# Performance work log

Measured on AMD Instinct MI355X. Metric: run time of the kernel, lower is better.

Reference implementation:

```python
import jax, jax.numpy as jnp
import numpy as np

B, T, D = 128, 2048, 256

def setup_inputs() -> dict:
    key = jax.random.key(0)
    k1, k2, k3, k4, k5 = jax.random.split(key, 5)
    h = jax.random.normal(k1, (B, D), dtype=jnp.float32)
    h_traj = jax.random.normal(k2, (B, T, D), dtype=jnp.float32)
    mask = jax.random.randint(k3, (B, T), 0, 2).astype(bool)  # True = masked
    # Linear(dim, 1) params (torch default init: U(-1/sqrt(D), 1/sqrt(D)))
    bound = 1.0 / np.sqrt(D)
    w = jax.random.uniform(k4, (D,), minval=-bound, maxval=bound, dtype=jnp.float32)
    b = jax.random.uniform(k5, (), minval=-bound, maxval=bound, dtype=jnp.float32)
    return {"h": h, "h_traj": h_traj, "mask": mask, "w": w, "b": b}

def reference(h, h_traj, mask, w, b):
    # score_bt = l1(h * h_traj) : broadcast multiply then dim->1 linear
    scores = jnp.einsum("bd,btd,d->bt", h, h_traj, w) + b          # [B, T]
    scores = jnp.where(mask, -jnp.inf, scores)
    beta = jax.nn.softmax(scores, axis=1)                           # [B, T]
    z = jnp.einsum("bt,btd->bd", beta, h_traj)                      # [B, D]
    return z
```

## Files before the change

### kernel.cpp

```cpp
#include <hip/hip_runtime.h>
#include <cstdint>

#define BB 128
#define TT 2048
#define DD 256
#define NCHUNK 8
#define TC (TT / NCHUNK)
#define NPART (BB * NCHUNK)


__global__ __launch_bounds__(256) void soft_att_partial(
    const float* __restrict__ h,
    const float* __restrict__ htraj,
    const int*   __restrict__ mask,
    const float* __restrict__ w,
    const float* __restrict__ bias,
    float* __restrict__ msv,
    float* __restrict__ lsv,
    float* __restrict__ zsv)
{
    const int blk  = blockIdx.x;
    const int b    = blk / NCHUNK;
    const int c    = blk % NCHUNK;
    const int tid  = threadIdx.x;
    const int lane = tid & 63;
    const int wv   = tid >> 6;
    const int g    = lane >> 4;
    const int i    = lane & 15;
    const int grp  = tid >> 4;

    const float* hb = h + (size_t)b * DD + i * 4;
    const float* wb = w + i * 4;
    float4 hw0, hw1, hw2, hw3;
    {
        float4 h0 = *(const float4*)(hb);       float4 w0 = *(const float4*)(wb);
        float4 h1 = *(const float4*)(hb + 64);  float4 w1 = *(const float4*)(wb + 64);
        float4 h2 = *(const float4*)(hb + 128); float4 w2 = *(const float4*)(wb + 128);
        float4 h3 = *(const float4*)(hb + 192); float4 w3 = *(const float4*)(wb + 192);
        hw0 = make_float4(h0.x*w0.x, h0.y*w0.y, h0.z*w0.z, h0.w*w0.w);
        hw1 = make_float4(h1.x*w1.x, h1.y*w1.y, h1.z*w1.z, h1.w*w1.w);
        hw2 = make_float4(h2.x*w2.x, h2.y*w2.y, h2.z*w2.z, h2.w*w2.w);
        hw3 = make_float4(h3.x*w3.x, h3.y*w3.y, h3.z*w3.z, h3.w*w3.w);
    }
    const float bscal = bias[0];

    const int t0 = c * TC + wv * 64;
    const int mk = mask[(size_t)b * TT + t0 + lane];
    unsigned long long bits = __ballot(mk == 0);

    const float* rowbase = htraj + ((size_t)b * TT + t0) * DD + i * 4;

    float m = -3.0e38f, l = 0.0f;
    float4 a0 = make_float4(0,0,0,0), a1 = a0, a2 = a0, a3 = a0;

    const int n = (int)((__popcll(bits) + 3) >> 2);

#define POP(r_, ok_) { \
    unsigned long long b0_ = bits; \
    unsigned long long b1_ = b0_ & (b0_ - 1); \
    unsigned long long b2_ = b1_ & (b1_ - 1); \
    unsigned long long b3_ = b2_ & (b2_ - 1); \
    int r0_ = b0_ ? __builtin_ctzll(b0_) : 0; \
    int r1_ = b1_ ? __builtin_ctzll(b1_) : 0; \
    int r2_ = b2_ ? __builtin_ctzll(b2_) : 0; \
    int r3_ = b3_ ? __builtin_ctzll(b3_) : 0; \
    bits = b3_ & (b3_ - 1); \
    r_  = (g & 2) ? ((g & 1) ? r3_ : r2_) : ((g & 1) ? r1_ : r0_); \
    ok_ = (g & 2) ? ((g & 1) ? (b3_ != 0) : (b2_ != 0)) \
                  : ((g & 1) ? (b1_ != 0) : (b0_ != 0)); }

#define LOADV(V0_, V1_, V2_, V3_, r_, ok_) { \
    if (ok_) { const float* p_ = rowbase + (size_t)(r_) * DD; \
        V0_ = *(const float4*)(p_); \
        V1_ = *(const float4*)(p_ + 64); \
        V2_ = *(const float4*)(p_ + 128); \
        V3_ = *(const float4*)(p_ + 192); } }

#define PROC(V0_, V1_, V2_, V3_, ok_) { \
    float s0_ = V0_.x*hw0.x; s0_ = fmaf(V0_.y,hw0.y,s0_); s0_ = fmaf(V0_.z,hw0.z,s0_); s0_ = fmaf(V0_.w,hw0.w,s0_); \
    float s1_ = V1_.x*hw1.x; s1_ = fmaf(V1_.y,hw1.y,s1_); s1_ = fmaf(V1_.z,hw1.z,s1_); s1_ = fmaf(V1_.w,hw1.w,s1_); \
    float s2_ = V2_.x*hw2.x; s2_ = fmaf(V2_.y,hw2.y,s2_); s2_ = fmaf(V2_.z,hw2.z,s2_); s2_ = fmaf(V2_.w,hw2.w,s2_); \
    float s3_ = V3_.x*hw3.x; s3_ = fmaf(V3_.y,hw3.y,s3_); s3_ = fmaf(V3_.z,hw3.z,s3_); s3_ = fmaf(V3_.w,hw3.w,s3_); \
    float s_ = (s0_ + s1_) + (s2_ + s3_); \
    s_ += __shfl_xor(s_, 1, 64); \
    s_ += __shfl_xor(s_, 2, 64); \
    s_ += __shfl_xor(s_, 4, 64); \
    s_ += __shfl_xor(s_, 8, 64); \
    s_ = (ok_) ? s_ + bscal : -INFINITY; \
    float mn_ = fmaxf(m, s_); \
    float sc_ = __expf(m - mn_); \
    float p_  = __expf(s_ - mn_); \
    a0.x = fmaf(a0.x, sc_, p_*V0_.x); a0.y = fmaf(a0.y, sc_, p_*V0_.y); \
    a0.z = fmaf(a0.z, sc_, p_*V0_.z); a0.w = fmaf(a0.w, sc_, p_*V0_.w); \
    a1.x = fmaf(a1.x, sc_, p_*V1_.x); a1.y = fmaf(a1.y, sc_, p_*V1_.y); \
    a1.z = fmaf(a1.z, sc_, p_*V1_.z); a1.w = fmaf(a1.w, sc_, p_*V1_.w); \
    a2.x = fmaf(a2.x, sc_, p_*V2_.x); a2.y = fmaf(a2.y, sc_, p_*V2_.y); \
    a2.z = fmaf(a2.z, sc_, p_*V2_.z); a2.w = fmaf(a2.w, sc_, p_*V2_.w); \
    a3.x = fmaf(a3.x, sc_, p_*V3_.x); a3.y = fmaf(a3.y, sc_, p_*V3_.y); \
    a3.z = fmaf(a3.z, sc_, p_*V3_.z); a3.w = fmaf(a3.w, sc_, p_*V3_.w); \
    l = fmaf(l, sc_, p_); m = mn_; }

    float4 A0 = make_float4(0,0,0,0), A1 = A0, A2 = A0, A3 = A0;
    float4 B0 = A0, B1 = A0, B2 = A0, B3 = A0;
    bool okA = false, okB = false;

    if (n > 0) { int r; POP(r, okA); LOADV(A0, A1, A2, A3, r, okA); }
    int it = 0;
    while (it < n) {
        if (it + 1 < n) { int r; POP(r, okB); LOADV(B0, B1, B2, B3, r, okB); }
        PROC(A0, A1, A2, A3, okA);
        if (++it >= n) break;
        if (it + 1 < n) { int r; POP(r, okA); LOADV(A0, A1, A2, A3, r, okA); }
        PROC(B0, B1, B2, B3, okB);
        if (++it >= n) break;
    }

    __shared__ float sm[16];
    __shared__ float sl[16];
    __shared__ float sz[16][DD];

    *(float4*)&sz[grp][i * 4      ] = a0;
    *(float4*)&sz[grp][i * 4 + 64 ] = a1;
    *(float4*)&sz[grp][i * 4 + 128] = a2;
    *(float4*)&sz[grp][i * 4 + 192] = a3;
    if (i == 0) { sm[grp] = m; sl[grp] = l; }
    __syncthreads();

    float M = -3.0e38f;
    #pragma unroll
    for (int k = 0; k < 16; ++k) M = fmaxf(M, sm[k]);
    float L = 0.f, Z = 0.f;
    #pragma unroll
    for (int k = 0; k < 16; ++k) {
        float e = __expf(sm[k] - M);
        L = fmaf(sl[k], e, L);
        Z = fmaf(sz[k][tid], e, Z);
    }
    if (tid == 0) { msv[blk] = M; lsv[blk] = L; }
    zsv[(size_t)blk * DD + tid] = Z;
#undef POP
#undef LOADV
#undef PROC
}

__global__ __launch_bounds__(128) void soft_att_combine(
    const float* __restrict__ msv,
    const float* __restrict__ lsv,
    const float* __restrict__ zsv,
    float* __restrict__ out)
{
    const int blk = blockIdx.x;
    const int b   = blk >> 1;
    const int d   = ((blk & 1) << 7) + threadIdx.x;

    float M = -3.0e38f;
    #pragma unroll
    for (int p = 0; p < NCHUNK; ++p)
        M = fmaxf(M, msv[b * NCHUNK + p]);

    float L = 0.f, Z = 0.f;
    #pragma unroll
    for (int p = 0; p < NCHUNK; ++p) {
        float e = __expf(msv[b * NCHUNK + p] - M);
        L = fmaf(lsv[b * NCHUNK + p], e, L);
        Z = fmaf(zsv[(size_t)(b * NCHUNK + p) * DD + d], e, Z);
    }
    out[(size_t)b * DD + d] = Z / L;
}

extern "C" void kernel_launch(void* const* d_in, const int* in_sizes, int n_in,
                              void* d_out, int out_size, void* d_ws, size_t ws_size,
                              hipStream_t stream) {
    const float* h     = (const float*)d_in[0];
    const float* htraj = (const float*)d_in[1];
    const int*   mask  = (const int*)d_in[2];
    const float* w     = (const float*)d_in[3];
    const float* bias  = (const float*)d_in[4];
    float* out = (float*)d_out;

    float* ms = (float*)d_ws;
    float* ls = ms + NPART;
    float* zs = ls + NPART;

    soft_att_partial<<<dim3(BB * NCHUNK), dim3(256), 0, stream>>>(
        h, htraj, mask, w, bias, ms, ls, zs);
    soft_att_combine<<<dim3(BB * 2), dim3(128), 0, stream>>>(ms, ls, zs, out);
}
```

Baseline: 30.80 us.

## Balance unmasked rows across all 16 groups via shared-memory compacted row lists

Instead of each wave popping bits from its own 64-row ballot, the block builds a compacted list of unmasked rows across all 256 rows in shared memory, interleaved so each of the 16 row-groups gets an equal share. This balances work across waves when mask density differs per wave and removes the per-iteration bit-popping arithmetic. It adds two block-level barriers and shared-memory prefix computation before the main loop.

```diff
diff --git a/kernel.cpp b/kernel.cpp
--- a/kernel.cpp
+++ b/kernel.cpp
@@ -8,6 +8,12 @@
 #define TC (TT / NCHUNK)
 #define NPART (BB * NCHUNK)
 
+
+__device__ __forceinline__ int rowOf(const uint4& lw, int s) {
+    unsigned word = (s & 8) ? ((s & 4) ? lw.w : lw.z)
+                            : ((s & 4) ? lw.y : lw.x);
+    return (int)((word >> ((s & 3) * 8)) & 255u);
+}
 
 __global__ __launch_bounds__(256) void soft_att_partial(
     const float* __restrict__ h,
@@ -25,7 +31,6 @@
     const int tid  = threadIdx.x;
     const int lane = tid & 63;
     const int wv   = tid >> 6;
-    const int g    = lane >> 4;
     const int i    = lane & 15;
     const int grp  = tid >> 4;
 
@@ -44,33 +49,39 @@
     }
     const float bscal = bias[0];
 
-    const int t0 = c * TC + wv * 64;
-    const int mk = mask[(size_t)b * TT + t0 + lane];
-    unsigned long long bits = __ballot(mk == 0);
-
-    const float* rowbase = htraj + ((size_t)b * TT + t0) * DD + i * 4;
+    __shared__ unsigned long long wballot[4];
+    __shared__ unsigned char lists[16][16];
+    __shared__ float sm[16];
+    __shared__ float sl[16];
+    __shared__ float sz[16][DD];
+
+    const int row = tid;
+    const int mk  = mask[(size_t)b * TT + c * TC + row];
+    unsigned long long bt = __ballot(mk == 0);
+    if (lane == 0) wballot[wv] = bt;
+    __syncthreads();
+    int prev = 0, tot = 0;
+    #pragma unroll
+    for (int k = 0; k < 4; ++k) {
+        int pc = __popcll(wballot[k]);
+        prev += (k < wv) ? pc : 0;
+        tot  += pc;
+    }
+    const int rank = prev + __popcll(bt & ((1ull << lane) - 1ull));
+    if (mk == 0) lists[rank & 15][rank >> 4] = (unsigned char)row;
+    __syncthreads();
+
+    const int cntmax = (tot + 15) >> 4;
+    const int mycnt  = (tot > grp) ? ((tot - grp + 15) >> 4) : 0;
+    const uint4 lw = *(const uint4*)&lists[grp][0];
+
+    const float* chunkbase = htraj + ((size_t)b * TT + c * TC) * DD + i * 4;
 
     float m = -3.0e38f, l = 0.0f;
     float4 a0 = make_float4(0,0,0,0), a1 = a0, a2 = a0, a3 = a0;
 
-    const int n = (int)((__popcll(bits) + 3) >> 2);
-
-#define POP(r_, ok_) { \
-    unsigned long long b0_ = bits; \
-    unsigned long long b1_ = b0_ & (b0_ - 1); \
-    unsigned long long b2_ = b1_ & (b1_ - 1); \
-    unsigned long long b3_ = b2_ & (b2_ - 1); \
-    int r0_ = b0_ ? __builtin_ctzll(b0_) : 0; \
-    int r1_ = b1_ ? __builtin_ctzll(b1_) : 0; \
-    int r2_ = b2_ ? __builtin_ctzll(b2_) : 0; \
-    int r3_ = b3_ ? __builtin_ctzll(b3_) : 0; \
-    bits = b3_ & (b3_ - 1); \
-    r_  = (g & 2) ? ((g & 1) ? r3_ : r2_) : ((g & 1) ? r1_ : r0_); \
-    ok_ = (g & 2) ? ((g & 1) ? (b3_ != 0) : (b2_ != 0)) \
-                  : ((g & 1) ? (b1_ != 0) : (b0_ != 0)); }
-
 #define LOADV(V0_, V1_, V2_, V3_, r_, ok_) { \
-    if (ok_) { const float* p_ = rowbase + (size_t)(r_) * DD; \
+    if (ok_) { const float* p_ = chunkbase + (size_t)(r_) * DD; \
         V0_ = *(const float4*)(p_); \
         V1_ = *(const float4*)(p_ + 64); \
         V2_ = *(const float4*)(p_ + 128); \
@@ -102,22 +113,24 @@
 
     float4 A0 = make_float4(0,0,0,0), A1 = A0, A2 = A0, A3 = A0;
     float4 B0 = A0, B1 = A0, B2 = A0, B3 = A0;
-    bool okA = false, okB = false;
-
-    if (n > 0) { int r; POP(r, okA); LOADV(A0, A1, A2, A3, r, okA); }
+
+    bool okA = (0 < mycnt), okB = false;
+    if (okA) { int r = rowOf(lw, 0); LOADV(A0, A1, A2, A3, r, okA); }
     int it = 0;
-    while (it < n) {
-        if (it + 1 < n) { int r; POP(r, okB); LOADV(B0, B1, B2, B3, r, okB); }
+    while (it < cntmax) {
+        if (it + 1 < cntmax) {
+            okB = (it + 1 < mycnt);
+            if (okB) { int r = rowOf(lw, it + 1); LOADV(B0, B1, B2, B3, r, okB); }
+        }
         PROC(A0, A1, A2, A3, okA);
-        if (++it >= n) break;
-        if (it + 1 < n) { int r; POP(r, okA); LOADV(A0, A1, A2, A3, r, okA); }
+        if (++it >= cntmax) break;
+        if (it + 1 < cntmax) {
+            okA = (it + 1 < mycnt);
+            if (okA) { int r = rowOf(lw, it + 1); LOADV(A0, A1, A2, A3, r, okA); }
+        }
         PROC(B0, B1, B2, B3, okB);
-        if (++it >= n) break;
-    }
-
-    __shared__ float sm[16];
-    __shared__ float sl[16];
-    __shared__ float sz[16][DD];
+        ++it;
+    }
 
     *(float4*)&sz[grp][i * 4      ] = a0;
     *(float4*)&sz[grp][i * 4 + 64 ] = a1;
@@ -138,7 +151,6 @@
     }
     if (tid == 0) { msv[blk] = M; lsv[blk] = L; }
     zsv[(size_t)blk * DD + tid] = Z;
-#undef POP
 #undef LOADV
 #undef PROC
 }
```

New measurement: 30.96 us. No clear change (+0.6%).
